# Kernel optimization log

Measured on AMD Instinct MI355X. Metric: run time of the kernel, lower is better.

## Reference

```python
import jax, jax.numpy as jnp
import numpy as np

HIDDEN = 1024
NUM_HEADS = 8
HEAD_DIM = HIDDEN // NUM_HEADS
ROPE_BASE = 10000.0
RMS_EPS = 1e-6


def _rotate_half(x):
    # interleaved rotate: (x0,x1,x2,x3,...) -> (-x1,x0,-x3,x2,...)
    x1 = x[..., ::2]
    x2 = x[..., 1::2]
    return jnp.stack([-x2, x1], axis=-1).reshape(x.shape)


def _rope_cos_sin(seq_len, rotary_dim, dtype):
    inv_freq = 1.0 / (ROPE_BASE ** (jnp.arange(0, rotary_dim, 2, dtype=jnp.float32) / rotary_dim))
    pos = jnp.arange(seq_len, dtype=jnp.float32)
    freqs = pos[:, None] * inv_freq[None, :]            # [S, rd/2]
    cos = jnp.repeat(jnp.cos(freqs), 2, axis=-1)        # [S, rd]
    sin = jnp.repeat(jnp.sin(freqs), 2, axis=-1)
    return cos.astype(dtype)[None, None], sin.astype(dtype)[None, None]


def setup_inputs() -> dict:
    key = jax.random.key(0)
    k = jax.random.split(key, 8)
    B, S, H = 2, 2048, HIDDEN
    hidden_states = jax.random.normal(k[0], (B, S, H), dtype=jnp.float32)
    attention_mask = jax.random.randint(k[1], (B, S, S), 0, 2) > 0
    rel_ts_bias = jax.random.normal(k[2], (B, S, S), dtype=jnp.float32)
    s1 = 1.0 / np.sqrt(H)
    W_qkvu = jax.random.normal(k[3], (H, H * 6), dtype=jnp.float32) * s1
    W_out = jax.random.normal(k[4], (H * 3, H), dtype=jnp.float32) * (1.0 / np.sqrt(H * 3))
    b_out = jnp.zeros((H,), dtype=jnp.float32)
    rms_weight = jnp.ones((H,), dtype=jnp.float32)
    return {"hidden_states": hidden_states, "attention_mask": attention_mask,
            "rel_ts_bias": rel_ts_bias, "W_qkvu": W_qkvu, "W_out": W_out,
            "b_out": b_out, "rms_weight": rms_weight}


def reference(hidden_states, attention_mask, rel_ts_bias, W_qkvu, W_out, b_out, rms_weight):
    B, S, H = hidden_states.shape
    nh, hd = NUM_HEADS, HEAD_DIM
    fused = jax.nn.silu(hidden_states @ W_qkvu)          # [B,S,6H]
    gated = fused[..., :3 * H]                            # [B,S,3H]
    v = fused[..., 3 * H:4 * H].reshape(B, S, nh, hd).transpose(0, 2, 1, 3)
    q = fused[..., 4 * H:5 * H].reshape(B, S, nh, hd).transpose(0, 2, 1, 3)
    kk = fused[..., 5 * H:].reshape(B, S, nh, hd).transpose(0, 2, 1, 3)

    cos, sin = _rope_cos_sin(S, hd, hidden_states.dtype)  # rotary_dim == head_dim
    q_rope = q * cos + _rotate_half(q) * sin
    k_rope = kk * cos + _rotate_half(kk) * sin

    inv_s = 1.0 / max(S, 1)
    qk = jax.nn.relu(jnp.einsum('bhnd,bhmd->bhnm', q, kk)) * inv_s
    qk_rope = jax.nn.relu(jnp.einsum('bhnd,bhmd->bhnm', q_rope, k_rope)) * inv_s

    mask = attention_mask[:, None]                        # [B,1,S,S]
    qk = jnp.where(mask, qk, 0.0)
    qk_rope = jnp.where(mask, qk_rope, 0.0)
    ts_bias = jnp.where(attention_mask, rel_ts_bias, 0.0)

    ts_out = jnp.einsum('bnm,bhmd->bnhd', ts_bias, v)
    rope_out = jnp.einsum('bhnm,bhmd->bnhd', qk_rope, v)
    plain_out = jnp.einsum('bhnm,bhmd->bnhd', qk, v)

    combined = jnp.concatenate([rope_out, ts_out, plain_out], axis=-1).reshape(B, S, 3 * H)
    out = (combined * gated) @ W_out + b_out
    y = out + hidden_states
    rms = jax.lax.rsqrt(jnp.mean(y * y, axis=-1, keepdims=True) + RMS_EPS)
    return y * rms * rms_weight
```

## Files before the change

### kernel.cpp

```cpp
#include <hip/hip_runtime.h>
#include <math.h>

static constexpr int Bz = 2;
static constexpr int Sq = 2048;
static constexpr int Hh = 1024;
static constexpr int NH = 8;
static constexpr int HD = 128;
static constexpr int H3 = 3072;
static constexpr int H6 = 6144;

typedef unsigned short ushort_t;
typedef float f32x4v __attribute__((ext_vector_type(4)));
typedef short s16x8 __attribute__((ext_vector_type(8)));

static constexpr size_t FUSED_OFF = 0;
static constexpr size_t A2_OFF    = 12582912;
static constexpr size_t HB_OFF    = 18874368;
static constexpr size_t MTB_OFF   = 18874368;
static constexpr size_t WQT_OFF   = 20971520;
static constexpr size_t WOT_OFF   = 24117248;
static constexpr size_t QR_OFF    = 25690112;
static constexpr size_t KR_OFF    = 27787264;
static constexpr size_t VT_OFF    = 29884416;
static constexpr size_t TAB_OFF   = 31981568;
static constexpr size_t FLAG_OFF  = 32243712;
static constexpr size_t TSB_OFF   = 32243716;

__device__ __forceinline__ float silu_(float x) { return x / (1.0f + expf(-x)); }
__device__ __forceinline__ ushort_t f2bf(float x) {
  unsigned int u = __float_as_uint(x);
  u += 0x7fffu + ((u >> 16) & 1u);
  return (ushort_t)(u >> 16);
}
__device__ __forceinline__ float bf2f(ushort_t u) {
  return __uint_as_float(((unsigned int)u) << 16);
}
__device__ __forceinline__ void g2l16(const ushort_t* g, ushort_t* l) {
  __builtin_amdgcn_global_load_lds(
      (const __attribute__((address_space(1))) unsigned int*)g,
      (__attribute__((address_space(3))) unsigned int*)l, 16, 0, 0);
}

__global__ __launch_bounds__(256) void hstu_mask_detect(const unsigned int* __restrict__ m,
                                                        int* __restrict__ flag) {
  __shared__ int s_any;
  if (threadIdx.x == 0) s_any = 0;
  __syncthreads();
  int any = 0;
  for (int i = threadIdx.x; i < 8192; i += 256)
    if (m[i] > 1u) any = 1;
  if (any) s_any = 1;
  __syncthreads();
  if (threadIdx.x == 0) *flag = s_any;
}

__global__ __launch_bounds__(256) void hstu_tab(float* __restrict__ tab) {
  int t = blockIdx.x * 256 + threadIdx.x;
  int i = t & 63;
  int s = t >> 6;
  float inv = powf(10000.0f, -(float)i / 64.0f);
  float sn, cs;
  sincosf((float)s * inv, &sn, &cs);
  tab[2 * t + 0] = cs;
  tab[2 * t + 1] = sn;
}

__global__ __launch_bounds__(256) void hstu_msk(const int* __restrict__ mask32,
                                                const unsigned char* __restrict__ mask8,
                                                const int* __restrict__ mflag,
                                                const float* __restrict__ bias,
                                                ushort_t* __restrict__ tsb,
                                                ushort_t* __restrict__ mtb) {
  const size_t base = ((size_t)blockIdx.x * 256 + threadIdx.x) * 8;
  const int m_u8 = *mflag;
  const ushort_t ivs = f2bf(1.0f / 2048.0f);
  int mk[8];
  if (m_u8) {
    uchar4 a = *(const uchar4*)&mask8[base];
    uchar4 b = *(const uchar4*)&mask8[base + 4];
    mk[0] = a.x; mk[1] = a.y; mk[2] = a.z; mk[3] = a.w;
    mk[4] = b.x; mk[5] = b.y; mk[6] = b.z; mk[7] = b.w;
  } else {
    int4 a = *(const int4*)&mask32[base];
    int4 b = *(const int4*)&mask32[base + 4];
    mk[0] = a.x; mk[1] = a.y; mk[2] = a.z; mk[3] = a.w;
    mk[4] = b.x; mk[5] = b.y; mk[6] = b.z; mk[7] = b.w;
  }
  float4 b0 = *(const float4*)&bias[base];
  float4 b1 = *(const float4*)&bias[base + 4];
  float bb[8] = {b0.x, b0.y, b0.z, b0.w, b1.x, b1.y, b1.z, b1.w};
  ushort_t ts[8], mt[8];
#pragma unroll
  for (int i = 0; i < 8; ++i) {
    ts[i] = f2bf(mk[i] ? bb[i] : 0.0f);
    mt[i] = mk[i] ? ivs : (ushort_t)0u;
  }
  *(s16x8*)&tsb[base] = *(s16x8*)ts;
  *(s16x8*)&mtb[base] = *(s16x8*)mt;
}

__global__ __launch_bounds__(256) void hstu_cvt(const float* __restrict__ in,
                                                ushort_t* __restrict__ out, int n4) {
  int i = blockIdx.x * 256 + threadIdx.x;
  if (i >= n4) return;
  float4 v = *(const float4*)&in[(size_t)i * 4];
  ushort4 o;
  o.x = f2bf(v.x); o.y = f2bf(v.y); o.z = f2bf(v.z); o.w = f2bf(v.w);
  *(ushort4*)&out[(size_t)i * 4] = o;
}

__global__ __launch_bounds__(256) void hstu_cvt_t(const float* __restrict__ in,
                                                  ushort_t* __restrict__ out, int K, int N) {
  __shared__ float t[32][33];
  const int n0 = blockIdx.x * 32, k0 = blockIdx.y * 32;
  const int c = threadIdx.x & 31, rr = threadIdx.x >> 5;
#pragma unroll
  for (int p = 0; p < 4; ++p)
    t[rr + p * 8][c] = in[(size_t)(k0 + rr + p * 8) * N + n0 + c];
  __syncthreads();
#pragma unroll
  for (int p = 0; p < 4; ++p)
    out[(size_t)(n0 + rr + p * 8) * K + k0 + c] = f2bf(t[c][rr + p * 8]);
}

__global__ __launch_bounds__(256) void hstu_rope(const ushort_t* __restrict__ fused,
                                                 const float2* __restrict__ tab,
                                                 ushort_t* __restrict__ qr,
                                                 ushort_t* __restrict__ kr) {
  const int idx = blockIdx.x * 256 + threadIdx.x;
  const int row = idx >> 7;
  const int cg = (idx & 127) * 8;
  const int s = row & (Sq - 1);
  const float2* trow = &tab[(size_t)s * 64 + ((cg & 127) >> 1)];
  float2 t[4];
#pragma unroll
  for (int p = 0; p < 4; ++p) t[p] = trow[p];

  s16x8 q8 = *(const s16x8*)&fused[(size_t)row * H6 + 4 * Hh + cg];
  s16x8 k8 = *(const s16x8*)&fused[(size_t)row * H6 + 5 * Hh + cg];
  ushort_t qo[8], ko[8];
#pragma unroll
  for (int p = 0; p < 4; ++p) {
    float qx = bf2f((ushort_t)q8[2 * p]), qy = bf2f((ushort_t)q8[2 * p + 1]);
    float kx = bf2f((ushort_t)k8[2 * p]), ky = bf2f((ushort_t)k8[2 * p + 1]);
    qo[2 * p] = f2bf(qx * t[p].x - qy * t[p].y);
    qo[2 * p + 1] = f2bf(qy * t[p].x + qx * t[p].y);
    ko[2 * p] = f2bf(kx * t[p].x - ky * t[p].y);
    ko[2 * p + 1] = f2bf(ky * t[p].x + kx * t[p].y);
  }
  *(s16x8*)&qr[(size_t)row * Hh + cg] = *(s16x8*)qo;
  *(s16x8*)&kr[(size_t)row * Hh + cg] = *(s16x8*)ko;
}

__global__ __launch_bounds__(256) void hstu_vt(const ushort_t* __restrict__ fused,
                                               ushort_t* __restrict__ vt) {
  __shared__ ushort_t t[32][36];
  const int m0 = blockIdx.x * 32, d0 = blockIdx.y * 32, bh = blockIdx.z;
  const int b = bh >> 3, h = bh & 7;
  const int r = threadIdx.x >> 3, cg = (threadIdx.x & 7) * 4;
  *(ushort4*)&t[r][cg] =
      *(const ushort4*)&fused[(size_t)(b * Sq + m0 + r) * H6 + 3 * Hh + h * HD + d0 + cg];
  __syncthreads();
  ushort4 o;
  o.x = t[cg + 0][r]; o.y = t[cg + 1][r]; o.z = t[cg + 2][r]; o.w = t[cg + 3][r];
  *(ushort4*)&vt[(size_t)(bh * HD + d0 + r) * Sq + m0 + cg] = o;
}

__global__ __launch_bounds__(256) void hstu_gemm_silu(const ushort_t* __restrict__ A,
                                                      const ushort_t* __restrict__ Bt,
                                                      ushort_t* __restrict__ C) {
  constexpr int K = 1024, N = H6;
  __shared__ ushort_t As[128 * 64];
  __shared__ ushort_t Bs[128 * 64];
  const int tid = threadIdx.x, lane = tid & 63, wid = tid >> 6;
  const int lo4 = lane & 15, hi2 = lane >> 4;
  const int wr = wid >> 1, wc = wid & 1;
  const int row0 = blockIdx.y * 128, col0 = blockIdx.x * 128;
  const int srow = lane >> 3, scol = (lane & 7) * 8;
  f32x4v acc[4][4];
#pragma unroll
  for (int i = 0; i < 4; ++i)
#pragma unroll
    for (int j = 0; j < 4; ++j) acc[i][j] = {0.f, 0.f, 0.f, 0.f};

  for (int k0 = 0; k0 < K; k0 += 64) {
    __syncthreads();
#pragma unroll
    for (int i = 0; i < 4; ++i) {
      const int rb = wid * 32 + i * 8;
      g2l16(&A[(size_t)(row0 + rb + srow) * K + k0 + scol], &As[rb * 64]);
      g2l16(&Bt[(size_t)(col0 + rb + srow) * K + k0 + scol], &Bs[rb * 64]);
    }
    __syncthreads();
#pragma unroll
    for (int kc = 0; kc < 2; ++kc) {
      s16x8 af[4], bfr[4];
#pragma unroll
      for (int mi = 0; mi < 4; ++mi)
        af[mi] = *(const s16x8*)&As[(wr * 64 + mi * 16 + lo4) * 64 + kc * 32 + hi2 * 8];
#pragma unroll
      for (int nj = 0; nj < 4; ++nj)
        bfr[nj] = *(const s16x8*)&Bs[(wc * 64 + nj * 16 + lo4) * 64 + kc * 32 + hi2 * 8];
#pragma unroll
      for (int mi = 0; mi < 4; ++mi)
#pragma unroll
        for (int nj = 0; nj < 4; ++nj)
          acc[mi][nj] = __builtin_amdgcn_mfma_f32_16x16x32_bf16(af[mi], bfr[nj], acc[mi][nj], 0, 0, 0);
    }
  }
#pragma unroll
  for (int mi = 0; mi < 4; ++mi)
#pragma unroll
    for (int nj = 0; nj < 4; ++nj)
#pragma unroll
      for (int r = 0; r < 4; ++r) {
        const int row = row0 + wr * 64 + mi * 16 + hi2 * 4 + r;
        const int col = col0 + wc * 64 + nj * 16 + lo4;
        C[(size_t)row * N + col] = f2bf(silu_(acc[mi][nj][r]));
      }
}

__global__ __launch_bounds__(256) void hstu_gemm_out(const ushort_t* __restrict__ A,
                                                     const ushort_t* __restrict__ Bt,
                                                     const float* __restrict__ bout,
                                                     const float* __restrict__ hidden,
                                                     float* __restrict__ C) {
  constexpr int K = H3, N = Hh;
  __shared__ ushort_t As[128 * 64];
  __shared__ ushort_t Bs[64 * 64];
  const int tid = threadIdx.x, lane = tid & 63, wid = tid >> 6;
  const int lo4 = lane & 15, hi2 = lane >> 4;
  const int wr = wid >> 1, wc = wid & 1;
  const int row0 = blockIdx.y * 128, col0 = blockIdx.x * 64;
  const int srow = lane >> 3, scol = (lane & 7) * 8;
  f32x4v acc[4][2];
#pragma unroll
  for (int i = 0; i < 4; ++i)
#pragma unroll
    for (int j = 0; j < 2; ++j) acc[i][j] = {0.f, 0.f, 0.f, 0.f};

  for (int k0 = 0; k0 < K; k0 += 64) {
    __syncthreads();
#pragma unroll
    for (int i = 0; i < 4; ++i) {
      const int rb = wid * 32 + i * 8;
      g2l16(&A[(size_t)(row0 + rb + srow) * K + k0 + scol], &As[rb * 64]);
    }
#pragma unroll
    for (int i = 0; i < 2; ++i) {
      const int rb = wid * 16 + i * 8;
      g2l16(&Bt[(size_t)(col0 + rb + srow) * K + k0 + scol], &Bs[rb * 64]);
    }
    __syncthreads();
#pragma unroll
    for (int kc = 0; kc < 2; ++kc) {
      s16x8 af[4], bfr[2];
#pragma unroll
      for (int mi = 0; mi < 4; ++mi)
        af[mi] = *(const s16x8*)&As[(wr * 64 + mi * 16 + lo4) * 64 + kc * 32 + hi2 * 8];
#pragma unroll
      for (int nj = 0; nj < 2; ++nj)
        bfr[nj] = *(const s16x8*)&Bs[(wc * 32 + nj * 16 + lo4) * 64 + kc * 32 + hi2 * 8];
#pragma unroll
      for (int mi = 0; mi < 4; ++mi)
#pragma unroll
        for (int nj = 0; nj < 2; ++nj)
          acc[mi][nj] = __builtin_amdgcn_mfma_f32_16x16x32_bf16(af[mi], bfr[nj], acc[mi][nj], 0, 0, 0);
    }
  }
#pragma unroll
  for (int mi = 0; mi < 4; ++mi)
#pragma unroll
    for (int nj = 0; nj < 2; ++nj)
#pragma unroll
      for (int r = 0; r < 4; ++r) {
        const int row = row0 + wr * 64 + mi * 16 + hi2 * 4 + r;
        const int col = col0 + wc * 32 + nj * 16 + lo4;
        C[(size_t)row * N + col] = acc[mi][nj][r] + bout[col] + hidden[(size_t)row * N + col];
      }
}

__global__ __launch_bounds__(512, 4) void hstu_attn(const ushort_t* __restrict__ fused,
                                                    const ushort_t* __restrict__ qr,
                                                    const ushort_t* __restrict__ kr,
                                                    const ushort_t* __restrict__ vt,
                                                    const ushort_t* __restrict__ tsb,
                                                    const ushort_t* __restrict__ mtb,
                                                    ushort_t* __restrict__ a2) {
  __shared__ __align__(16) ushort_t Ks[32][136];
  __shared__ __align__(16) ushort_t KRs[32][136];
  __shared__ __align__(16) ushort_t Vt[128][40];
  __shared__ __align__(16) ushort_t Pl[3][64][40];
  __shared__ __align__(16) ushort_t Mt[64][40];

  const int tid = threadIdx.x;
  const int lane = tid & 63;
  const int wid = tid >> 6;
  const int lo4 = lane & 15;
  const int hi2 = lane >> 4;
  const int h = blockIdx.x;
  const int n0 = blockIdx.y * 64;
  const int b = blockIdx.z;

  const int krow = tid >> 4, kcol = (tid & 15) * 8;
  const int vdd = tid >> 2, vmg = (tid & 3) * 8;
  const int trow = (tid & 255) >> 2, tmg = (tid & 3) * 8;
  const ushort_t* TM = (wid < 4) ? tsb : mtb;
  const size_t kbase = (size_t)b * Sq * H6 + 5 * Hh + h * HD + kcol;
  const size_t krbase = (size_t)b * Sq * Hh + h * HD + kcol;
  const size_t vbase = (size_t)((b * NH + h) * HD + vdd) * Sq + vmg;
  const size_t tbase = (size_t)(b * Sq + n0 + trow) * Sq + tmg;

  const int t_w = wid >> 2;
  const int rq = wid & 3;
  s16x8 qf[4];
  {
    const int row = tid >> 4;
    const int colg = (tid & 15) * 8;
#pragma unroll
    for (int half = 0; half < 2; ++half) {
      const size_t gr = (size_t)(b * Sq + n0 + half * 32 + row);
      *(s16x8*)&Ks[row][colg] = *(const s16x8*)&fused[gr * H6 + 4 * Hh + h * HD + colg];
      *(s16x8*)&KRs[row][colg] = *(const s16x8*)&qr[gr * Hh + h * HD + colg];
      __syncthreads();
      if ((rq >> 1) == half) {
        const int lrow = (rq & 1) * 16 + lo4;
        const ushort_t(*Qsrc)[136] = t_w ? KRs : Ks;
#pragma unroll
        for (int c = 0; c < 4; ++c)
          qf[c] = *(const s16x8*)&Qsrc[lrow][c * 32 + hi2 * 8];
      }
      __syncthreads();
    }
  }

  const f32x4v zero4 = {0.f, 0.f, 0.f, 0.f};
  f32x4v accO[3][2][2];
#pragma unroll
  for (int t = 0; t < 3; ++t)
#pragma unroll
    for (int rt = 0; rt < 2; ++rt)
#pragma unroll
      for (int ct = 0; ct < 2; ++ct) accO[t][rt][ct] = zero4;

  const int rh2 = wid >> 2;
  const int cq = wid & 3;

  s16x8 kreg, krreg, vreg, tmreg;
#define LOADT(T)                                                            \
  {                                                                         \
    const size_t moff = (size_t)(T) * 32;                                   \
    kreg = *(const s16x8*)&fused[kbase + (moff + krow) * H6];               \
    krreg = *(const s16x8*)&kr[krbase + (moff + krow) * Hh];                \
    vreg = *(const s16x8*)&vt[vbase + moff];                                \
    tmreg = *(const s16x8*)&TM[tbase + moff];                               \
  }
#define WRITET()                                                            \
  {                                                                         \
    *(s16x8*)&Ks[krow][kcol] = kreg;                                        \
    *(s16x8*)&KRs[krow][kcol] = krreg;                                      \
    *(s16x8*)&Vt[vdd][vmg] = vreg;                                          \
    if (wid < 4) *(s16x8*)&Pl[2][trow][tmg] = tmreg;                        \
    else *(s16x8*)&Mt[trow][tmg] = tmreg;                                   \
  }

  LOADT(0);
  WRITET();
  __syncthreads();

  for (int t = 0; t < Sq / 32; ++t) {
    if (t + 1 < Sq / 32) LOADT(t + 1);
    {
      const ushort_t(*Kmat)[136] = t_w ? KRs : Ks;
      const int n = rq * 16 + lo4;
#pragma unroll
      for (int mt2 = 0; mt2 < 2; ++mt2) {
        f32x4v a = zero4;
#pragma unroll
        for (int c = 0; c < 4; ++c) {
          s16x8 kf = *(const s16x8*)&Kmat[mt2 * 16 + lo4][c * 32 + hi2 * 8];
          a = __builtin_amdgcn_mfma_f32_16x16x32_bf16(kf, qf[c], a, 0, 0, 0);
        }
        const int mb = mt2 * 16 + hi2 * 4;
        ushort4 mt4 = *(const ushort4*)&Mt[n][mb];
        ushort4 po;
        po.x = f2bf(fmaxf(a[0], 0.f) * bf2f(mt4.x));
        po.y = f2bf(fmaxf(a[1], 0.f) * bf2f(mt4.y));
        po.z = f2bf(fmaxf(a[2], 0.f) * bf2f(mt4.z));
        po.w = f2bf(fmaxf(a[3], 0.f) * bf2f(mt4.w));
        *(ushort4*)&Pl[t_w][n][mb] = po;
      }
    }
    __syncthreads();
    {
      s16x8 af[3][2];
#pragma unroll
      for (int ty = 0; ty < 3; ++ty)
#pragma unroll
        for (int rt = 0; rt < 2; ++rt)
          af[ty][rt] = *(const s16x8*)&Pl[ty][rh2 * 32 + rt * 16 + lo4][hi2 * 8];
      s16x8 bfv[2];
#pragma unroll
      for (int ct = 0; ct < 2; ++ct)
        bfv[ct] = *(const s16x8*)&Vt[cq * 32 + ct * 16 + lo4][hi2 * 8];
#pragma unroll
      for (int ty = 0; ty < 3; ++ty)
#pragma unroll
        for (int rt = 0; rt < 2; ++rt)
#pragma unroll
          for (int ct = 0; ct < 2; ++ct)
            accO[ty][rt][ct] =
                __builtin_amdgcn_mfma_f32_16x16x32_bf16(af[ty][rt], bfv[ct], accO[ty][rt][ct], 0, 0, 0);
    }
    __syncthreads();
    if (t + 1 < Sq / 32) WRITET();
    __syncthreads();
  }
#undef LOADT
#undef WRITET

  const int toff[3] = {256, 0, 128};
#pragma unroll
  for (int ty = 0; ty < 3; ++ty)
#pragma unroll
    for (int rt = 0; rt < 2; ++rt)
#pragma unroll
      for (int ct = 0; ct < 2; ++ct)
#pragma unroll
        for (int r = 0; r < 4; ++r) {
          const int n = n0 + rh2 * 32 + rt * 16 + hi2 * 4 + r;
          const int dd = cq * 32 + ct * 16 + lo4;
          const int col3 = h * 384 + toff[ty] + dd;
          const float g = bf2f(fused[(size_t)(b * Sq + n) * H6 + col3]);
          a2[(size_t)(b * Sq + n) * H3 + col3] = f2bf(accO[ty][rt][ct][r] * g);
        }
}

__global__ __launch_bounds__(256) void hstu_rms(float* __restrict__ y,
                                                const float* __restrict__ w) {
  __shared__ float red[4];
  const int row = blockIdx.x;
  const int tid = threadIdx.x;
  float4 v = *(float4*)&y[(size_t)row * Hh + tid * 4];
  float ss = v.x * v.x + v.y * v.y + v.z * v.z + v.w * v.w;
#pragma unroll
  for (int o = 32; o > 0; o >>= 1) ss += __shfl_down(ss, o);
  if ((tid & 63) == 0) red[tid >> 6] = ss;
  __syncthreads();
  const float tot = red[0] + red[1] + red[2] + red[3];
  const float r = 1.0f / sqrtf(tot / (float)Hh + 1e-6f);
  float4 wv = *(const float4*)&w[tid * 4];
  v.x *= r * wv.x;
  v.y *= r * wv.y;
  v.z *= r * wv.z;
  v.w *= r * wv.w;
  *(float4*)&y[(size_t)row * Hh + tid * 4] = v;
}

extern "C" void kernel_launch(void* const* d_in, const int* in_sizes, int n_in,
                              void* d_out, int out_size, void* d_ws, size_t ws_size,
                              hipStream_t stream) {
  const float* hidden = (const float*)d_in[0];
  const void* mask = d_in[1];
  const float* bias = (const float*)d_in[2];
  const float* Wqkvu = (const float*)d_in[3];
  const float* Wout = (const float*)d_in[4];
  const float* bout = (const float*)d_in[5];
  const float* rmsw = (const float*)d_in[6];
  float* out = (float*)d_out;
  float* ws = (float*)d_ws;

  ushort_t* fused = (ushort_t*)(ws + FUSED_OFF);
  ushort_t* a2 = (ushort_t*)(ws + A2_OFF);
  ushort_t* hb = (ushort_t*)(ws + HB_OFF);
  ushort_t* mtbp = (ushort_t*)(ws + MTB_OFF);
  ushort_t* wqt = (ushort_t*)(ws + WQT_OFF);
  ushort_t* wot = (ushort_t*)(ws + WOT_OFF);
  ushort_t* qrb = (ushort_t*)(ws + QR_OFF);
  ushort_t* krb = (ushort_t*)(ws + KR_OFF);
  ushort_t* vtb = (ushort_t*)(ws + VT_OFF);
  float* tab = ws + TAB_OFF;
  int* mflag = (int*)(ws + FLAG_OFF);
  ushort_t* tsbp = (ushort_t*)(ws + TSB_OFF);

  hstu_mask_detect<<<1, 256, 0, stream>>>((const unsigned int*)mask, mflag);
  hstu_tab<<<512, 256, 0, stream>>>(tab);
  hstu_cvt<<<4096, 256, 0, stream>>>(hidden, hb, (Bz * Sq * Hh) / 4);
  hstu_cvt_t<<<dim3(H6 / 32, Hh / 32), 256, 0, stream>>>(Wqkvu, wqt, Hh, H6);
  hstu_cvt_t<<<dim3(Hh / 32, H3 / 32), 256, 0, stream>>>(Wout, wot, H3, Hh);
  hstu_gemm_silu<<<dim3(H6 / 128, (Bz * Sq) / 128), 256, 0, stream>>>(hb, wqt, fused);
  hstu_msk<<<(Bz * Sq * Sq / 8) / 256, 256, 0, stream>>>(
      (const int*)mask, (const unsigned char*)mask, mflag, bias, tsbp, mtbp);
  hstu_rope<<<(Bz * Sq * Hh / 8) / 256, 256, 0, stream>>>(fused, (const float2*)tab, qrb, krb);
  hstu_vt<<<dim3(Sq / 32, HD / 32, Bz * NH), 256, 0, stream>>>(fused, vtb);
  hstu_attn<<<dim3(NH, Sq / 64, Bz), 512, 0, stream>>>(fused, qrb, krb, vtb, tsbp, mtbp, a2);
  hstu_gemm_out<<<dim3(Hh / 64, (Bz * Sq) / 128), 256, 0, stream>>>(a2, wot, bout, hidden, out);
  hstu_rms<<<Bz * Sq, 256, 0, stream>>>(out, rmsw);
}
```

Before: 331.0 us.

## Merge small prep kernels and double-buffer V/ts tiles in attention loop

```diff
diff --git a/kernel.cpp b/kernel.cpp
--- a/kernel.cpp
+++ b/kernel.cpp
@@ -41,20 +41,21 @@
       (__attribute__((address_space(3))) unsigned int*)l, 16, 0, 0);
 }
 
-__global__ __launch_bounds__(256) void hstu_mask_detect(const unsigned int* __restrict__ m,
-                                                        int* __restrict__ flag) {
+__global__ __launch_bounds__(256) void hstu_pre(const unsigned int* __restrict__ m,
+                                                int* __restrict__ flag,
+                                                float* __restrict__ tab) {
   __shared__ int s_any;
-  if (threadIdx.x == 0) s_any = 0;
-  __syncthreads();
-  int any = 0;
-  for (int i = threadIdx.x; i < 8192; i += 256)
-    if (m[i] > 1u) any = 1;
-  if (any) s_any = 1;
-  __syncthreads();
-  if (threadIdx.x == 0) *flag = s_any;
-}
-
-__global__ __launch_bounds__(256) void hstu_tab(float* __restrict__ tab) {
+  if (blockIdx.x == 512) {
+    if (threadIdx.x == 0) s_any = 0;
+    __syncthreads();
+    int any = 0;
+    for (int i = threadIdx.x; i < 8192; i += 256)
+      if (m[i] > 1u) any = 1;
+    if (any) s_any = 1;
+    __syncthreads();
+    if (threadIdx.x == 0) *flag = s_any;
+    return;
+  }
   int t = blockIdx.x * 256 + threadIdx.x;
   int i = t & 63;
   int s = t >> 6;
@@ -99,70 +100,85 @@
   *(s16x8*)&mtb[base] = *(s16x8*)mt;
 }
 
-__global__ __launch_bounds__(256) void hstu_cvt(const float* __restrict__ in,
-                                                ushort_t* __restrict__ out, int n4) {
-  int i = blockIdx.x * 256 + threadIdx.x;
-  if (i >= n4) return;
-  float4 v = *(const float4*)&in[(size_t)i * 4];
-  ushort4 o;
-  o.x = f2bf(v.x); o.y = f2bf(v.y); o.z = f2bf(v.z); o.w = f2bf(v.w);
-  *(ushort4*)&out[(size_t)i * 4] = o;
-}
-
-__global__ __launch_bounds__(256) void hstu_cvt_t(const float* __restrict__ in,
-                                                  ushort_t* __restrict__ out, int K, int N) {
-  __shared__ float t[32][33];
-  const int n0 = blockIdx.x * 32, k0 = blockIdx.y * 32;
+__global__ __launch_bounds__(256) void hstu_cvt_all(const float* __restrict__ hidden,
+                                                    ushort_t* __restrict__ hb,
+                                                    const float* __restrict__ Wq,
+                                                    ushort_t* __restrict__ wqt,
+                                                    const float* __restrict__ Wo,
+                                                    ushort_t* __restrict__ wot) {
+  __shared__ float tbuf[32][33];
+  const int blk = blockIdx.x;
+  if (blk < 4096) {
+    const int idx = blk * 256 + threadIdx.x;
+    float4 v = *(const float4*)&hidden[(size_t)idx * 4];
+    ushort4 o;
+    o.x = f2bf(v.x); o.y = f2bf(v.y); o.z = f2bf(v.z); o.w = f2bf(v.w);
+    *(ushort4*)&hb[(size_t)idx * 4] = o;
+    return;
+  }
+  const float* in;
+  ushort_t* out;
+  int K, N, n0, k0;
+  if (blk < 4096 + 6144) {
+    const int j = blk - 4096;
+    in = Wq; out = wqt; K = 1024; N = 6144;
+    n0 = (j % 192) * 32; k0 = (j / 192) * 32;
+  } else {
+    const int j = blk - 10240;
+    in = Wo; out = wot; K = 3072; N = 1024;
+    n0 = (j % 32) * 32; k0 = (j / 32) * 32;
+  }
   const int c = threadIdx.x & 31, rr = threadIdx.x >> 5;
 #pragma unroll
   for (int p = 0; p < 4; ++p)
-    t[rr + p * 8][c] = in[(size_t)(k0 + rr + p * 8) * N + n0 + c];
+    tbuf[rr + p * 8][c] = in[(size_t)(k0 + rr + p * 8) * N + n0 + c];
   __syncthreads();
 #pragma unroll
   for (int p = 0; p < 4; ++p)
-    out[(size_t)(n0 + rr + p * 8) * K + k0 + c] = f2bf(t[c][rr + p * 8]);
-}
-
-__global__ __launch_bounds__(256) void hstu_rope(const ushort_t* __restrict__ fused,
-                                                 const float2* __restrict__ tab,
-                                                 ushort_t* __restrict__ qr,
-                                                 ushort_t* __restrict__ kr) {
-  const int idx = blockIdx.x * 256 + threadIdx.x;
-  const int row = idx >> 7;
-  const int cg = (idx & 127) * 8;
-  const int s = row & (Sq - 1);
-  const float2* trow = &tab[(size_t)s * 64 + ((cg & 127) >> 1)];
-  float2 t[4];
-#pragma unroll
-  for (int p = 0; p < 4; ++p) t[p] = trow[p];
-
-  s16x8 q8 = *(const s16x8*)&fused[(size_t)row * H6 + 4 * Hh + cg];
-  s16x8 k8 = *(const s16x8*)&fused[(size_t)row * H6 + 5 * Hh + cg];
-  ushort_t qo[8], ko[8];
-#pragma unroll
-  for (int p = 0; p < 4; ++p) {
-    float qx = bf2f((ushort_t)q8[2 * p]), qy = bf2f((ushort_t)q8[2 * p + 1]);
-    float kx = bf2f((ushort_t)k8[2 * p]), ky = bf2f((ushort_t)k8[2 * p + 1]);
-    qo[2 * p] = f2bf(qx * t[p].x - qy * t[p].y);
-    qo[2 * p + 1] = f2bf(qy * t[p].x + qx * t[p].y);
-    ko[2 * p] = f2bf(kx * t[p].x - ky * t[p].y);
-    ko[2 * p + 1] = f2bf(ky * t[p].x + kx * t[p].y);
-  }
-  *(s16x8*)&qr[(size_t)row * Hh + cg] = *(s16x8*)qo;
-  *(s16x8*)&kr[(size_t)row * Hh + cg] = *(s16x8*)ko;
-}
-
-__global__ __launch_bounds__(256) void hstu_vt(const ushort_t* __restrict__ fused,
-                                               ushort_t* __restrict__ vt) {
-  __shared__ ushort_t t[32][36];
-  const int m0 = blockIdx.x * 32, d0 = blockIdx.y * 32, bh = blockIdx.z;
+    out[(size_t)(n0 + rr + p * 8) * K + k0 + c] = f2bf(tbuf[c][rr + p * 8]);
+}
+
+__global__ __launch_bounds__(256) void hstu_prep2(const ushort_t* __restrict__ fused,
+                                                  const float2* __restrict__ tab,
+                                                  ushort_t* __restrict__ qr,
+                                                  ushort_t* __restrict__ kr,
+                                                  ushort_t* __restrict__ vt) {
+  __shared__ ushort_t tbuf[32][36];
+  const int blk = blockIdx.x;
+  if (blk < 2048) {
+    const int idx = blk * 256 + threadIdx.x;
+    const int row = idx >> 7;
+    const int cg = (idx & 127) * 8;
+    const int s = row & (Sq - 1);
+    const float2* trow = &tab[(size_t)s * 64 + ((cg & 127) >> 1)];
+    float2 t[4];
+#pragma unroll
+    for (int p = 0; p < 4; ++p) t[p] = trow[p];
+    s16x8 q8 = *(const s16x8*)&fused[(size_t)row * H6 + 4 * Hh + cg];
+    s16x8 k8 = *(const s16x8*)&fused[(size_t)row * H6 + 5 * Hh + cg];
+    ushort_t qo[8], ko[8];
+#pragma unroll
+    for (int p = 0; p < 4; ++p) {
+      float qx = bf2f((ushort_t)q8[2 * p]), qy = bf2f((ushort_t)q8[2 * p + 1]);
+      float kx = bf2f((ushort_t)k8[2 * p]), ky = bf2f((ushort_t)k8[2 * p + 1]);
+      qo[2 * p] = f2bf(qx * t[p].x - qy * t[p].y);
+      qo[2 * p + 1] = f2bf(qy * t[p].x + qx * t[p].y);
+      ko[2 * p] = f2bf(kx * t[p].x - ky * t[p].y);
+      ko[2 * p + 1] = f2bf(ky * t[p].x + kx * t[p].y);
+    }
+    *(s16x8*)&qr[(size_t)row * Hh + cg] = *(s16x8*)qo;
+    *(s16x8*)&kr[(size_t)row * Hh + cg] = *(s16x8*)ko;
+    return;
+  }
+  const int j = blk - 2048;
+  const int m0 = (j & 63) * 32, d0 = ((j >> 6) & 3) * 32, bh = j >> 8;
   const int b = bh >> 3, h = bh & 7;
   const int r = threadIdx.x >> 3, cg = (threadIdx.x & 7) * 4;
-  *(ushort4*)&t[r][cg] =
+  *(ushort4*)&tbuf[r][cg] =
       *(const ushort4*)&fused[(size_t)(b * Sq + m0 + r) * H6 + 3 * Hh + h * HD + d0 + cg];
   __syncthreads();
   ushort4 o;
-  o.x = t[cg + 0][r]; o.y = t[cg + 1][r]; o.z = t[cg + 2][r]; o.w = t[cg + 3][r];
+  o.x = tbuf[cg + 0][r]; o.y = tbuf[cg + 1][r]; o.z = tbuf[cg + 2][r]; o.w = tbuf[cg + 3][r];
   *(ushort4*)&vt[(size_t)(bh * HD + d0 + r) * Sq + m0 + cg] = o;
 }
 
@@ -289,8 +305,9 @@
                                                     ushort_t* __restrict__ a2) {
   __shared__ __align__(16) ushort_t Ks[32][136];
   __shared__ __align__(16) ushort_t KRs[32][136];
-  __shared__ __align__(16) ushort_t Vt[128][40];
-  __shared__ __align__(16) ushort_t Pl[3][64][40];
+  __shared__ __align__(16) ushort_t Vt[2][128][40];
+  __shared__ __align__(16) ushort_t Pl[2][64][40];
+  __shared__ __align__(16) ushort_t Pts[2][64][40];
   __shared__ __align__(16) ushort_t Mt[64][40];
 
   const int tid = threadIdx.x;
@@ -301,6 +318,7 @@
   const int h = blockIdx.x;
   const int n0 = blockIdx.y * 64;
   const int b = blockIdx.z;
+  constexpr int NT = Sq / 32;
 
   const int krow = tid >> 4, kcol = (tid & 15) * 8;
   const int vdd = tid >> 2, vmg = (tid & 3) * 8;
@@ -355,21 +373,22 @@
     vreg = *(const s16x8*)&vt[vbase + moff];                                \
     tmreg = *(const s16x8*)&TM[tbase + moff];                               \
   }
-#define WRITET()                                                            \
+#define WRITET(BUF)                                                         \
   {                                                                         \
     *(s16x8*)&Ks[krow][kcol] = kreg;                                        \
     *(s16x8*)&KRs[krow][kcol] = krreg;                                      \
-    *(s16x8*)&Vt[vdd][vmg] = vreg;                                          \
-    if (wid < 4) *(s16x8*)&Pl[2][trow][tmg] = tmreg;                        \
+    *(s16x8*)&Vt[BUF][vdd][vmg] = vreg;                                     \
+    if (wid < 4) *(s16x8*)&Pts[BUF][trow][tmg] = tmreg;                     \
     else *(s16x8*)&Mt[trow][tmg] = tmreg;                                   \
   }
 
   LOADT(0);
-  WRITET();
+  WRITET(0);
   __syncthreads();
 
-  for (int t = 0; t < Sq / 32; ++t) {
-    if (t + 1 < Sq / 32) LOADT(t + 1);
+  for (int t = 0; t < NT; ++t) {
+    const int cur = t & 1;
+    if (t + 1 < NT) LOADT(t + 1);
     {
       const ushort_t(*Kmat)[136] = t_w ? KRs : Ks;
       const int n = rq * 16 + lo4;
@@ -395,14 +414,16 @@
     {
       s16x8 af[3][2];
 #pragma unroll
-      for (int ty = 0; ty < 3; ++ty)
-#pragma unroll
-        for (int rt = 0; rt < 2; ++rt)
-          af[ty][rt] = *(const s16x8*)&Pl[ty][rh2 * 32 + rt * 16 + lo4][hi2 * 8];
+      for (int rt = 0; rt < 2; ++rt) {
+        af[0][rt] = *(const s16x8*)&Pl[0][rh2 * 32 + rt * 16 + lo4][hi2 * 8];
+        af[1][rt] = *(const s16x8*)&Pl[1][rh2 * 32 + rt * 16 + lo4][hi2 * 8];
+        af[2][rt] = *(const s16x8*)&Pts[cur][rh2 * 32 + rt * 16 + lo4][hi2 * 8];
+      }
       s16x8 bfv[2];
 #pragma unroll
       for (int ct = 0; ct < 2; ++ct)
-        bfv[ct] = *(const s16x8*)&Vt[cq * 32 + ct * 16 + lo4][hi2 * 8];
+        bfv[ct] = *(const s16x8*)&Vt[cur][cq * 32 + ct * 16 + lo4][hi2 * 8];
+      if (t + 1 < NT) WRITET(cur ^ 1);
 #pragma unroll
       for (int ty = 0; ty < 3; ++ty)
 #pragma unroll
@@ -412,8 +433,6 @@
             accO[ty][rt][ct] =
                 __builtin_amdgcn_mfma_f32_16x16x32_bf16(af[ty][rt], bfv[ct], accO[ty][rt][ct], 0, 0, 0);
     }
-    __syncthreads();
-    if (t + 1 < Sq / 32) WRITET();
     __syncthreads();
   }
 #undef LOADT
@@ -483,16 +502,12 @@
   int* mflag = (int*)(ws + FLAG_OFF);
   ushort_t* tsbp = (ushort_t*)(ws + TSB_OFF);
 
-  hstu_mask_detect<<<1, 256, 0, stream>>>((const unsigned int*)mask, mflag);
-  hstu_tab<<<512, 256, 0, stream>>>(tab);
-  hstu_cvt<<<4096, 256, 0, stream>>>(hidden, hb, (Bz * Sq * Hh) / 4);
-  hstu_cvt_t<<<dim3(H6 / 32, Hh / 32), 256, 0, stream>>>(Wqkvu, wqt, Hh, H6);
-  hstu_cvt_t<<<dim3(Hh / 32, H3 / 32), 256, 0, stream>>>(Wout, wot, H3, Hh);
+  hstu_pre<<<513, 256, 0, stream>>>((const unsigned int*)mask, mflag, tab);
+  hstu_cvt_all<<<13312, 256, 0, stream>>>(hidden, hb, Wqkvu, wqt, Wout, wot);
   hstu_gemm_silu<<<dim3(H6 / 128, (Bz * Sq) / 128), 256, 0, stream>>>(hb, wqt, fused);
   hstu_msk<<<(Bz * Sq * Sq / 8) / 256, 256, 0, stream>>>(
       (const int*)mask, (const unsigned char*)mask, mflag, bias, tsbp, mtbp);
-  hstu_rope<<<(Bz * Sq * Hh / 8) / 256, 256, 0, stream>>>(fused, (const float2*)tab, qrb, krb);
-  hstu_vt<<<dim3(Sq / 32, HD / 32, Bz * NH), 256, 0, stream>>>(fused, vtb);
+  hstu_prep2<<<6144, 256, 0, stream>>>(fused, (const float2*)tab, qrb, krb, vtb);
   hstu_attn<<<dim3(NH, Sq / 64, Bz), 512, 0, stream>>>(fused, qrb, krb, vtb, tsbp, mtbp, a2);
   hstu_gemm_out<<<dim3(Hh / 64, (Bz * Sq) / 128), 256, 0, stream>>>(a2, wot, bout, hidden, out);
   hstu_rms<<<Bz * Sq, 256, 0, stream>>>(out, rmsw);
```

Result: no change. 327.6 us (-1.0%).
